# Performance work log

Hardware: AMD Instinct MI355X
Metric: run time of the kernel (lower is better)

## Reference

```python
import jax, jax.numpy as jnp
import numpy as np

MAX_RADIUS = 0.9
TEMP = 0.1

def _to_poincare(x, W, b):
    # Linear + Tanh, then rescale into Poincare ball of radius 0.9
    h = jnp.tanh(x @ W.T + b)
    norm = jnp.clip(jnp.linalg.norm(h, axis=-1, keepdims=True), 1e-8, None)
    scale = jnp.where(norm > MAX_RADIUS, MAX_RADIUS / norm, jnp.ones_like(norm))
    return h * scale

def setup_inputs() -> dict:
    key = jax.random.key(0)
    kq, kw, kb, km, ko = jax.random.split(key, 5)
    B, N, D = 2048, 100000, 128
    return {
        "query": jax.random.normal(kq, (B, D), dtype=jnp.float32),
        "W": jax.random.normal(kw, (D, D), dtype=jnp.float32) * (1.0 / np.sqrt(D)),
        "b": jax.random.normal(kb, (D,), dtype=jnp.float32) * 0.01,
        "mem_emb": jax.random.normal(km, (N, D), dtype=jnp.float32),
        "mem_out": jax.random.normal(ko, (N, D), dtype=jnp.float32),
        "k": 16,
    }

def reference(query, W, b, mem_emb, mem_out, k):
    q = _to_poincare(query, W, b)          # [B, D]
    m = _to_poincare(mem_emb, W, b)        # [N, D]
    # Euclidean cdist via the GEMM form: ||q||^2 + ||m||^2 - 2 q.m
    q2 = jnp.sum(q * q, axis=-1, keepdims=True)           # [B, 1]
    m2 = jnp.sum(m * m, axis=-1)                          # [N]
    d2 = q2 + m2[None, :] - 2.0 * (q @ m.T)               # [B, N]
    dists = jnp.sqrt(jnp.maximum(d2, 1e-12))
    # k smallest distances
    neg_top, top_idx = jax.lax.top_k(-dists, k)           # [B, k]
    top_dists = -neg_top
    weights = jax.nn.softmax(-top_dists / TEMP, axis=-1)  # [B, k]
    outcomes = mem_out[top_idx]                           # [B, k, D]
    return weights, outcomes
```

## Files before the change

### kernel.cpp

```cpp
#include <hip/hip_runtime.h>
#include <hip/hip_bf16.h>
#include <math.h>

#define DIM 128
#define QB 128
#define MB 64
#define NSPLIT 32
#define KSEL 16
#define KOWN 4
#define RESCORE 32
#define IDXMASK 0x1FFFu
#define KEYMASK 0xFFFFE000u
#define M2MAX 3200

using bf16x8 = __attribute__((ext_vector_type(8))) short;
using f32x4  = __attribute__((ext_vector_type(4))) float;

__device__ inline unsigned short f2bf(float f) {
  __hip_bfloat16 h = __float2bfloat16(f);
  return __builtin_bit_cast(unsigned short, h);
}
__device__ inline unsigned uminu(unsigned a, unsigned b) {
  return __builtin_elementwise_min(a, b);
}
__device__ inline unsigned umaxu(unsigned a, unsigned b) {
  return __builtin_elementwise_max(a, b);
}
__device__ inline unsigned umed3(unsigned a, unsigned b, unsigned c) {
  unsigned r;
  asm("v_med3_u32 %0, %1, %2, %3" : "=v"(r) : "v"(a), "v"(b), "v"(c));
  return r;
}
__device__ inline unsigned long long umin64(unsigned long long a,
                                            unsigned long long b) {
  return __builtin_elementwise_min(a, b);
}

__device__ inline f32x4 mfma16(bf16x8 a, bf16x8 b, f32x4 c) {
  return __builtin_amdgcn_mfma_f32_16x16x32_bf16(a, b, c, 0, 0, 0);
}

__device__ inline void gload_lds16(const void* g, void* l) {
  __builtin_amdgcn_global_load_lds(
      (const __attribute__((address_space(1))) void*)g,
      (__attribute__((address_space(3))) void*)l, 16, 0, 0);
}

__device__ inline void ins4(unsigned (&ks)[KOWN], unsigned c) {
  const unsigned n0 = uminu(c, ks[0]);
  const unsigned n1 = umed3(c, ks[0], ks[1]);
  const unsigned n2 = umed3(c, ks[1], ks[2]);
  const unsigned n3 = umed3(c, ks[2], ks[3]);
  ks[0] = n0; ks[1] = n1; ks[2] = n2; ks[3] = n3;
}

__global__ __launch_bounds__(512) void poincare2_k(
    const float* __restrict__ Xm, int Rm,
    const float* __restrict__ Xq, int Rq,
    const float* __restrict__ W, const float* __restrict__ bias,
    float* __restrict__ Pm, float* __restrict__ Pm2,
    float* __restrict__ Pm2s, int npadm,
    unsigned short* __restrict__ Pmbf,
    float* __restrict__ Pq, float* __restrict__ Pq2, int nbm)
{
  __shared__ float Wl[DIM * DIM];
  __shared__ float nrm[128 * 17];
  __shared__ float norm2l[128];

  const int t  = threadIdx.x;
  const int cg = t & 15;
  const int rg = t >> 4;

  const bool ismem = (int)blockIdx.x < nbm;
  const float* X = ismem ? Xm : Xq;
  const int    R = ismem ? Rm : Rq;
  float*       P  = ismem ? Pm  : Pq;
  float*       P2 = ismem ? Pm2 : Pq2;
  unsigned short* Pbf = ismem ? Pmbf : nullptr;
  const int rbase = (ismem ? blockIdx.x : (blockIdx.x - nbm)) * 128;

  for (int i = t; i < DIM * 32; i += 512) {
    const int j = i >> 5, c = i & 31;
    const float4 v = *(const float4*)&W[j * DIM + c * 4];
    *(float4*)&Wl[j * DIM + ((c ^ ((j >> 3) & 7)) << 2)] = v;
  }
  float bj[8];
  #pragma unroll
  for (int u = 0; u < 8; ++u) bj[u] = bias[cg * 8 + u];

  const float* xr[4];
  #pragma unroll
  for (int v = 0; v < 4; ++v) {
    int row = rbase + rg + 32 * v;
    if (row > R - 1) row = R - 1;
    xr[v] = X + (size_t)row * DIM;
  }
  __syncthreads();

  float acc[4][8];
  #pragma unroll
  for (int v = 0; v < 4; ++v)
    #pragma unroll
    for (int u = 0; u < 8; ++u) acc[v][u] = bj[u];

  #pragma unroll 2
  for (int k4 = 0; k4 < 32; ++k4) {
    float4 xv[4], wv[8];
    #pragma unroll
    for (int v = 0; v < 4; ++v) xv[v] = *(const float4*)&xr[v][k4 * 4];
    #pragma unroll
    for (int u = 0; u < 8; ++u) {
      const int j = cg * 8 + u;
      wv[u] = *(const float4*)&Wl[j * DIM + ((k4 ^ ((j >> 3) & 7)) << 2)];
    }
    #pragma unroll
    for (int v = 0; v < 4; ++v)
      #pragma unroll
      for (int u = 0; u < 8; ++u) {
        acc[v][u] = fmaf(xv[v].x, wv[u].x, acc[v][u]);
        acc[v][u] = fmaf(xv[v].y, wv[u].y, acc[v][u]);
        acc[v][u] = fmaf(xv[v].z, wv[u].z, acc[v][u]);
        acc[v][u] = fmaf(xv[v].w, wv[u].w, acc[v][u]);
      }
  }

  #pragma unroll
  for (int v = 0; v < 4; ++v) {
    float pn = 0.f;
    #pragma unroll
    for (int u = 0; u < 8; ++u) {
      const float th = tanhf(acc[v][u]);
      acc[v][u] = th;
      pn = fmaf(th, th, pn);
    }
    nrm[(rg + 32 * v) * 17 + cg] = pn;
  }
  __syncthreads();
  if (t < 128) {
    float s = 0.f;
    #pragma unroll
    for (int c2 = 0; c2 < 16; ++c2) s += nrm[t * 17 + c2];
    norm2l[t] = s;
    const int row = rbase + t;
    if (row < R) {
      const float nm = sqrtf(s);
      const float sc = (nm > 0.9f) ? (0.9f / nm) : 1.0f;
      const float p2v = s * sc * sc;
      P2[row] = p2v;
      if (ismem) Pm2s[row] = fmaf(0.5f, p2v, 1.0f);
    } else if (ismem && row < npadm) {
      Pm2s[row] = __int_as_float(0x7f800000);
    }
  }
  __syncthreads();

  #pragma unroll
  for (int v = 0; v < 4; ++v) {
    const int r = rg + 32 * v;
    const int row = rbase + r;
    if (row < R) {
      const float n2 = norm2l[r];
      const float nm = sqrtf(n2);
      const float sc = (nm > 0.9f) ? (0.9f / nm) : 1.0f;
      float o[8];
      #pragma unroll
      for (int u = 0; u < 8; ++u) o[u] = acc[v][u] * sc;
      *(float4*)&P[(size_t)row * DIM + cg * 8]     = make_float4(o[0], o[1], o[2], o[3]);
      *(float4*)&P[(size_t)row * DIM + cg * 8 + 4] = make_float4(o[4], o[5], o[6], o[7]);
      if (Pbf) {
        uint4 pb;
        pb.x = (unsigned)f2bf(o[0]) | ((unsigned)f2bf(o[1]) << 16);
        pb.y = (unsigned)f2bf(o[2]) | ((unsigned)f2bf(o[3]) << 16);
        pb.z = (unsigned)f2bf(o[4]) | ((unsigned)f2bf(o[5]) << 16);
        pb.w = (unsigned)f2bf(o[6]) | ((unsigned)f2bf(o[7]) << 16);
        *(uint4*)&Pmbf[(size_t)row * DIM + ((cg ^ (row & 15)) << 3)] = pb;
      }
    }
  }
}

template<bool USEBF>
__global__ __launch_bounds__(512, 2) void score_topk_k(
    const float* __restrict__ Pq,
    const float* __restrict__ Pm, const float* __restrict__ Pm2s,
    const unsigned short* __restrict__ Pmbf,
    int N, int splitlen, unsigned* __restrict__ splitTop)
{
  __shared__ __align__(16) unsigned short Ml[3][MB * DIM];
  __shared__ float m2all[M2MAX];

  const int t = threadIdx.x;
  const int lane = t & 63;
  const int w = t >> 6, wr = w >> 1, wc = w & 1;
  const int split = blockIdx.x;
  const int qbase = blockIdx.y * QB;
  const int mlo = split * splitlen;
  const int mhi = min(mlo + splitlen, N);
  const int ntiles = (mhi - mlo + MB - 1) / MB;

  bf16x8 qf[2][4];
  #pragma unroll
  for (int s = 0; s < 2; ++s) {
    const int qrow = qbase + wr * 32 + s * 16 + (lane & 15);
    #pragma unroll
    for (int ks = 0; ks < 4; ++ks) {
      const float* src = &Pq[(size_t)qrow * DIM + ks * 32 + (lane >> 4) * 8];
      float4 lo = *(const float4*)src;
      float4 hi = *(const float4*)(src + 4);
      bf16x8 v;
      v[0] = (short)f2bf(-lo.x); v[1] = (short)f2bf(-lo.y);
      v[2] = (short)f2bf(-lo.z); v[3] = (short)f2bf(-lo.w);
      v[4] = (short)f2bf(-hi.x); v[5] = (short)f2bf(-hi.y);
      v[6] = (short)f2bf(-hi.z); v[7] = (short)f2bf(-hi.w);
      qf[s][ks] = v;
    }
  }

  for (int i = t; i < splitlen; i += 512) m2all[i] = Pm2s[mlo + i];

  const size_t soff0 = (size_t)(w * 8 + (lane >> 4)) * DIM + ((lane & 15) << 3);
  const size_t soff1 = soff0 + 4 * DIM;

  auto stageU = [&](int tilei, int buf) {
    const unsigned short* b = Pmbf + (size_t)(mlo + tilei * MB) * DIM;
    gload_lds16(b + soff0, &Ml[buf][(w * 8) * DIM]);
    gload_lds16(b + soff1, &Ml[buf][(w * 8 + 4) * DIM]);
  };
  uint4 sv0, sv1;
  auto stageF_load = [&](int tilei) {
    const int fr = t >> 3, fe = t & 7;
    const float* src = Pm + (size_t)(mlo + tilei * MB + fr) * DIM + fe * 16;
    float4 a0 = *(const float4*)(src + 0);
    float4 a1 = *(const float4*)(src + 4);
    float4 a2 = *(const float4*)(src + 8);
    float4 a3 = *(const float4*)(src + 12);
    sv0.x = (unsigned)f2bf(a0.x) | ((unsigned)f2bf(a0.y) << 16);
    sv0.y = (unsigned)f2bf(a0.z) | ((unsigned)f2bf(a0.w) << 16);
    sv0.z = (unsigned)f2bf(a1.x) | ((unsigned)f2bf(a1.y) << 16);
    sv0.w = (unsigned)f2bf(a1.z) | ((unsigned)f2bf(a1.w) << 16);
    sv1.x = (unsigned)f2bf(a2.x) | ((unsigned)f2bf(a2.y) << 16);
    sv1.y = (unsigned)f2bf(a2.z) | ((unsigned)f2bf(a2.w) << 16);
    sv1.z = (unsigned)f2bf(a3.x) | ((unsigned)f2bf(a3.y) << 16);
    sv1.w = (unsigned)f2bf(a3.z) | ((unsigned)f2bf(a3.w) << 16);
  };
  auto stageF_write = [&](int buf) {
    const int fr = t >> 3, fe = t & 7;
    char* base = (char*)&Ml[buf][0] + fr * 256;
    *(uint4*)(base + (((2 * fe)     ^ (fr & 15)) << 4)) = sv0;
    *(uint4*)(base + (((2 * fe + 1) ^ (fr & 15)) << 4)) = sv1;
  };

  unsigned keys[2][4][KOWN];
  #pragma unroll
  for (int s = 0; s < 2; ++s)
    #pragma unroll
    for (int r = 0; r < 4; ++r)
      #pragma unroll
      for (int i = 0; i < KOWN; ++i) keys[s][r][i] = 0xFFFFFFFFu;

  const int mcol = wc * 32 + (lane & 15);
  const int rowA = mcol, rowB = mcol + 16;

  auto compute = [&](int tile, const unsigned short* cur) {
    const float ca = m2all[tile * MB + mcol];
    const float cb = m2all[tile * MB + mcol + 16];
    f32x4 a00 = (f32x4){ca, ca, ca, ca};
    f32x4 a01 = (f32x4){cb, cb, cb, cb};
    f32x4 a10 = (f32x4){ca, ca, ca, ca};
    f32x4 a11 = (f32x4){cb, cb, cb, cb};
    __builtin_amdgcn_s_setprio(1);
    #pragma unroll
    for (int ks = 0; ks < 4; ++ks) {
      const int kb = ks * 64 + (lane >> 4) * 16;
      bf16x8 bfrA = *(const bf16x8*)((const char*)cur + rowA * 256 +
                                     (kb ^ ((rowA & 15) << 4)));
      bf16x8 bfrB = *(const bf16x8*)((const char*)cur + rowB * 256 +
                                     (kb ^ ((rowB & 15) << 4)));
      a00 = mfma16(qf[0][ks], bfrA, a00);
      a01 = mfma16(qf[0][ks], bfrB, a01);
      a10 = mfma16(qf[1][ks], bfrA, a10);
      a11 = mfma16(qf[1][ks], bfrB, a11);
    }
    __builtin_amdgcn_s_setprio(0);
    const unsigned idx0 = (unsigned)(tile * MB + mcol);
    #pragma unroll
    for (int r = 0; r < 4; ++r) {
      ins4(keys[0][r], (__float_as_uint(a00[r]) & KEYMASK) | idx0);
      ins4(keys[0][r], (__float_as_uint(a01[r]) & KEYMASK) | (idx0 + 16));
      ins4(keys[1][r], (__float_as_uint(a10[r]) & KEYMASK) | idx0);
      ins4(keys[1][r], (__float_as_uint(a11[r]) & KEYMASK) | (idx0 + 16));
    }
  };

  if constexpr (USEBF) {
    __syncthreads();
    stageU(0, 0);
    if (ntiles > 1) stageU(1, 1);
    int cur = 0;
    for (int i = 0; i < ntiles; ++i) {
      if (i < ntiles - 1) asm volatile("s_waitcnt vmcnt(2)" ::: "memory");
      else                asm volatile("s_waitcnt vmcnt(0)" ::: "memory");
      __builtin_amdgcn_s_barrier();
      __builtin_amdgcn_sched_barrier(0);
      int nb = cur + 2; if (nb >= 3) nb -= 3;
      if (i + 2 < ntiles) stageU(i + 2, nb);
      compute(i, &Ml[cur][0]);
      cur = (cur + 1 == 3) ? 0 : cur + 1;
    }
  } else {
    stageF_load(0);
    stageF_write(0);
    __syncthreads();
    for (int i = 0; i < ntiles; ++i) {
      const int cur = i & 1;
      const bool more = (i + 1 < ntiles);
      if (more) stageF_load(i + 1);
      compute(i, &Ml[cur][0]);
      __syncthreads();
      if (more) stageF_write(cur ^ 1);
      __syncthreads();
    }
  }

  unsigned* mb = (unsigned*)&Ml[0][0];
  __syncthreads();
  #pragma unroll
  for (int s = 0; s < 2; ++s)
    #pragma unroll
    for (int r = 0; r < 4; ++r) {
      unsigned k0 = keys[s][r][0], k1 = keys[s][r][1];
      unsigned k2 = keys[s][r][2], k3 = keys[s][r][3];
      unsigned out = 0xFFFFFFFFu;
      for (int round = 0; round < 8; ++round) {
        unsigned g = k0;
        g = uminu(g, __shfl_xor(g, 1, 16));
        g = uminu(g, __shfl_xor(g, 2, 16));
        g = uminu(g, __shfl_xor(g, 4, 16));
        g = uminu(g, __shfl_xor(g, 8, 16));
        const bool mine = (k0 == g);
        k0 = mine ? k1 : k0;
        k1 = mine ? k2 : k1;
        k2 = mine ? k3 : k2;
        k3 = mine ? 0xFFFFFFFFu : k3;
        if ((lane & 15) == round) out = g;
      }
      const int lq = wr * 32 + s * 16 + (lane >> 4) * 4 + r;
      if ((lane & 15) < 8) mb[lq * 16 + wc * 8 + (lane & 15)] = out;
    }
  __syncthreads();
  if (wc == 0 && lane < 32) {
    const int lq = wr * 32 + lane;
    unsigned s8[8];
    #pragma unroll
    for (int i = 0; i < 8; ++i) s8[i] = 0xFFFFFFFFu;
    const unsigned* src = mb + lq * 16;
    #pragma unroll
    for (int i = 0; i < 16; ++i) {
      const unsigned c = src[i];
      const unsigned n0 = uminu(c, s8[0]);
      const unsigned n1 = umed3(c, s8[0], s8[1]);
      const unsigned n2 = umed3(c, s8[1], s8[2]);
      const unsigned n3 = umed3(c, s8[2], s8[3]);
      const unsigned n4 = umed3(c, s8[3], s8[4]);
      const unsigned n5 = umed3(c, s8[4], s8[5]);
      const unsigned n6 = umed3(c, s8[5], s8[6]);
      const unsigned n7 = umed3(c, s8[6], s8[7]);
      s8[0] = n0; s8[1] = n1; s8[2] = n2; s8[3] = n3;
      s8[4] = n4; s8[5] = n5; s8[6] = n6; s8[7] = n7;
    }
    unsigned* dst = &splitTop[((size_t)(qbase + lq) * NSPLIT + split) * 8];
    *(uint4*)dst       = make_uint4(s8[0], s8[1], s8[2], s8[3]);
    *((uint4*)dst + 1) = make_uint4(s8[4], s8[5], s8[6], s8[7]);
  }
}

__global__ __launch_bounds__(256) void finalize_k(
    const unsigned* __restrict__ splitTop,
    const float* __restrict__ Pq, const float* __restrict__ Pq2,
    const float* __restrict__ Pm, const float* __restrict__ Pm2,
    const float* __restrict__ memOut, int N, int splitlen,
    float* __restrict__ outW, float* __restrict__ outO)
{
  const int wv   = threadIdx.x >> 6;
  const int lane = threadIdx.x & 63;
  const int q = blockIdx.x * 4 + wv;

  __shared__ unsigned      sKey[4][RESCORE];
  __shared__ unsigned char sSrc[4][RESCORE];
  __shared__ unsigned long long sKeyx[4][RESCORE];
  __shared__ unsigned long long sSel[4][KSEL];
  __shared__ float sEl[4][KSEL];

  {
    unsigned a[8];
    if (lane < NSPLIT) {
      const unsigned* gp = splitTop + (size_t)q * (NSPLIT * 8) + lane * 8;
      uint4 lo = *(const uint4*)gp;
      uint4 hi = *(const uint4*)(gp + 4);
      a[0] = lo.x; a[1] = lo.y; a[2] = lo.z; a[3] = lo.w;
      a[4] = hi.x; a[5] = hi.y; a[6] = hi.z; a[7] = hi.w;
    } else {
      #pragma unroll
      for (int i = 0; i < 8; ++i) a[i] = 0xFFFFFFFFu;
    }
    for (int r = 0; r < RESCORE; ++r) {
      unsigned g = a[0];
      g = uminu(g, __shfl_xor(g, 1));
      g = uminu(g, __shfl_xor(g, 2));
      g = uminu(g, __shfl_xor(g, 4));
      g = uminu(g, __shfl_xor(g, 8));
      g = uminu(g, __shfl_xor(g, 16));
      g = uminu(g, __shfl_xor(g, 32));
      unsigned long long mask = __ballot(a[0] == g);
      const int fl = __ffsll((unsigned long long)mask) - 1;
      if (lane == fl) {
        #pragma unroll
        for (int i = 0; i < 7; ++i) a[i] = a[i + 1];
        a[7] = 0xFFFFFFFFu;
      }
      if (lane == 0) { sKey[wv][r] = g; sSrc[wv][r] = (unsigned char)fl; }
    }
  }

  #pragma unroll
  for (int p = 0; p < 4; ++p) {
    const int g8 = p * 8 + (lane >> 3), e = lane & 7;
    const int gidx = (int)sSrc[wv][g8] * splitlen + (int)(sKey[wv][g8] & IDXMASK);
    const float4* qr = (const float4*)&Pq[(size_t)q * DIM];
    const float4* mr = (const float4*)&Pm[(size_t)gidx * DIM];
    float s = 0.f;
    #pragma unroll
    for (int u = 0; u < 4; ++u) {
      float4 a = qr[e * 4 + u], b = mr[e * 4 + u];
      s = fmaf(a.x, b.x, s); s = fmaf(a.y, b.y, s);
      s = fmaf(a.z, b.z, s); s = fmaf(a.w, b.w, s);
    }
    s += __shfl_xor(s, 1, 8);
    s += __shfl_xor(s, 2, 8);
    s += __shfl_xor(s, 4, 8);
    if (e == 0) {
      float d2 = (Pq2[q] + Pm2[gidx]) - 2.0f * s;
      float dist = sqrtf(fmaxf(d2, 1e-12f));
      sKeyx[wv][g8] =
          (((unsigned long long)__float_as_uint(dist)) << 32) | (unsigned)gidx;
    }
  }

  {
    unsigned long long kk = (lane < RESCORE) ? sKeyx[wv][lane] : ~0ull;
    for (int r = 0; r < KSEL; ++r) {
      unsigned long long g = kk;
      g = umin64(g, __shfl_xor(g, 1));
      g = umin64(g, __shfl_xor(g, 2));
      g = umin64(g, __shfl_xor(g, 4));
      g = umin64(g, __shfl_xor(g, 8));
      g = umin64(g, __shfl_xor(g, 16));
      g = umin64(g, __shfl_xor(g, 32));
      if (kk == g) kk = ~0ull;
      if (lane == 0) sSel[wv][r] = g;
    }
  }

  if (lane < KSEL) {
    const float d  = __uint_as_float((unsigned)(sSel[wv][lane] >> 32));
    const float d0 = __uint_as_float((unsigned)(sSel[wv][0] >> 32));
    sEl[wv][lane] = expf((d0 - d) * 10.0f);
  }
  if (lane < KSEL) {
    float sum = 0.f;
    #pragma unroll
    for (int i = 0; i < KSEL; ++i) sum += sEl[wv][i];
    outW[(size_t)q * KSEL + lane] = sEl[wv][lane] / sum;
  }

  #pragma unroll
  for (int i = 0; i < 8; ++i) {
    const int f4 = lane + i * 64;
    const int r = f4 >> 5, c4 = f4 & 31;
    const int idx = (int)(sSel[wv][r] & 0xffffffffu);
    *(float4*)&outO[((size_t)q * KSEL + r) * DIM + c4 * 4] =
        *(const float4*)&memOut[(size_t)idx * DIM + c4 * 4];
  }
}

extern "C" void kernel_launch(void* const* d_in, const int* in_sizes, int n_in,
                              void* d_out, int out_size, void* d_ws, size_t ws_size,
                              hipStream_t stream)
{
  const float* query   = (const float*)d_in[0];
  const float* W       = (const float*)d_in[1];
  const float* bias    = (const float*)d_in[2];
  const float* mem_emb = (const float*)d_in[3];
  const float* mem_out = (const float*)d_in[4];
  const int B = in_sizes[0] / DIM;
  const int N = in_sizes[3] / DIM;

  const int splitlen = ((N + NSPLIT * MB - 1) / (NSPLIT * MB)) * MB;
  const int N_pad2 = NSPLIT * splitlen;

  float* ws  = (float*)d_ws;
  float* Pm  = ws;
  float* Pm2 = Pm + (size_t)N * DIM;
  float* Pm2s = Pm2 + N;
  float* Pq  = Pm2s + N_pad2;
  float* Pq2 = Pq + (size_t)B * DIM;
  unsigned* splitTop = (unsigned*)(Pq2 + B);
  unsigned short* Pmbf = (unsigned short*)(splitTop + (size_t)B * NSPLIT * 8);
  const size_t need_bf = (size_t)((char*)(Pmbf + (size_t)N_pad2 * DIM) - (char*)d_ws);
  const bool usebf = ws_size >= need_bf;

  float* outW = (float*)d_out;
  float* outO = outW + (size_t)B * KSEL;

  const int nbm = (N_pad2 + 127) / 128;
  const int nbq = (B + 127) / 128;
  poincare2_k<<<dim3(nbm + nbq), dim3(512), 0, stream>>>(
      mem_emb, N, query, B, W, bias, Pm, Pm2, Pm2s, N_pad2,
      usebf ? Pmbf : nullptr, Pq, Pq2, nbm);

  dim3 grid2(NSPLIT, B / QB);
  if (usebf)
    score_topk_k<true><<<grid2, dim3(512), 0, stream>>>(Pq, Pm, Pm2s, Pmbf, N,
                                                        splitlen, splitTop);
  else
    score_topk_k<false><<<grid2, dim3(512), 0, stream>>>(Pq, Pm, Pm2s, nullptr, N,
                                                         splitlen, splitTop);

  finalize_k<<<dim3(B / 4), dim3(256), 0, stream>>>(splitTop, Pq, Pq2, Pm, Pm2,
                                                    mem_out, N, splitlen,
                                                    outW, outO);
}
```

Baseline: 191.3 us.

## Retile Poincare projection kernel to 256 rows per block with shuffle norm reduction

Result: slower. 225.2 us (+17.8%).

```diff
diff --git a/kernel.cpp b/kernel.cpp
--- a/kernel.cpp
+++ b/kernel.cpp
@@ -54,7 +54,7 @@
   ks[0] = n0; ks[1] = n1; ks[2] = n2; ks[3] = n3;
 }
 
-__global__ __launch_bounds__(512) void poincare2_k(
+__global__ __launch_bounds__(512, 2) void poincare2_k(
     const float* __restrict__ Xm, int Rm,
     const float* __restrict__ Xq, int Rq,
     const float* __restrict__ W, const float* __restrict__ bias,
@@ -64,12 +64,10 @@
     float* __restrict__ Pq, float* __restrict__ Pq2, int nbm)
 {
   __shared__ float Wl[DIM * DIM];
-  __shared__ float nrm[128 * 17];
-  __shared__ float norm2l[128];
-
-  const int t  = threadIdx.x;
-  const int cg = t & 15;
-  const int rg = t >> 4;
+
+  const int t   = threadIdx.x;
+  const int cg  = t & 15;
+  const int rg2 = t >> 4;
 
   const bool ismem = (int)blockIdx.x < nbm;
   const float* X = ismem ? Xm : Xq;
@@ -77,94 +75,92 @@
   float*       P  = ismem ? Pm  : Pq;
   float*       P2 = ismem ? Pm2 : Pq2;
   unsigned short* Pbf = ismem ? Pmbf : nullptr;
-  const int rbase = (ismem ? blockIdx.x : (blockIdx.x - nbm)) * 128;
+  const int rbase = (ismem ? blockIdx.x : (blockIdx.x - nbm)) * 256;
+  const int r0 = rbase + rg2 * 8;
 
   for (int i = t; i < DIM * 32; i += 512) {
     const int j = i >> 5, c = i & 31;
     const float4 v = *(const float4*)&W[j * DIM + c * 4];
     *(float4*)&Wl[j * DIM + ((c ^ ((j >> 3) & 7)) << 2)] = v;
   }
-  float bj[8];
-  #pragma unroll
-  for (int u = 0; u < 8; ++u) bj[u] = bias[cg * 8 + u];
-
-  const float* xr[4];
-  #pragma unroll
-  for (int v = 0; v < 4; ++v) {
-    int row = rbase + rg + 32 * v;
-    if (row > R - 1) row = R - 1;
-    xr[v] = X + (size_t)row * DIM;
-  }
+
+  unsigned xoff[8];
+  #pragma unroll
+  for (int i = 0; i < 8; ++i) {
+    int row = r0 + i; if (row > R - 1) row = R - 1;
+    xoff[i] = (unsigned)row * (DIM * 4);
+  }
+
+  float acc[8][8];
+  #pragma unroll
+  for (int i = 0; i < 8; ++i)
+    #pragma unroll
+    for (int u = 0; u < 8; ++u) acc[i][u] = bias[cg * 8 + u];
   __syncthreads();
 
-  float acc[4][8];
-  #pragma unroll
-  for (int v = 0; v < 4; ++v)
-    #pragma unroll
-    for (int u = 0; u < 8; ++u) acc[v][u] = bj[u];
-
+  const float* Wb = &Wl[(cg * 8) * DIM];
+  const int sw = (cg & 7) << 2;
   #pragma unroll 2
   for (int k4 = 0; k4 < 32; ++k4) {
-    float4 xv[4], wv[8];
-    #pragma unroll
-    for (int v = 0; v < 4; ++v) xv[v] = *(const float4*)&xr[v][k4 * 4];
+    float4 xv[8];
+    #pragma unroll
+    for (int i = 0; i < 8; ++i)
+      xv[i] = *(const float4*)((const char*)X + xoff[i] + k4 * 16);
+    const int wch = ((k4 << 2) ^ sw);
     #pragma unroll
     for (int u = 0; u < 8; ++u) {
-      const int j = cg * 8 + u;
-      wv[u] = *(const float4*)&Wl[j * DIM + ((k4 ^ ((j >> 3) & 7)) << 2)];
-    }
-    #pragma unroll
-    for (int v = 0; v < 4; ++v)
+      const float4 wvv = *(const float4*)(Wb + u * DIM + wch);
       #pragma unroll
-      for (int u = 0; u < 8; ++u) {
-        acc[v][u] = fmaf(xv[v].x, wv[u].x, acc[v][u]);
-        acc[v][u] = fmaf(xv[v].y, wv[u].y, acc[v][u]);
-        acc[v][u] = fmaf(xv[v].z, wv[u].z, acc[v][u]);
-        acc[v][u] = fmaf(xv[v].w, wv[u].w, acc[v][u]);
+      for (int i = 0; i < 8; ++i) {
+        acc[i][u] = fmaf(xv[i].x, wvv.x, acc[i][u]);
+        acc[i][u] = fmaf(xv[i].y, wvv.y, acc[i][u]);
+        acc[i][u] = fmaf(xv[i].z, wvv.z, acc[i][u]);
+        acc[i][u] = fmaf(xv[i].w, wvv.w, acc[i][u]);
       }
-  }
-
-  #pragma unroll
-  for (int v = 0; v < 4; ++v) {
-    float pn = 0.f;
+    }
+  }
+
+  float pn[8];
+  #pragma unroll
+  for (int i = 0; i < 8; ++i) {
+    float p = 0.f;
     #pragma unroll
     for (int u = 0; u < 8; ++u) {
-      const float th = tanhf(acc[v][u]);
-      acc[v][u] = th;
-      pn = fmaf(th, th, pn);
-    }
-    nrm[(rg + 32 * v) * 17 + cg] = pn;
-  }
-  __syncthreads();
-  if (t < 128) {
-    float s = 0.f;
-    #pragma unroll
-    for (int c2 = 0; c2 < 16; ++c2) s += nrm[t * 17 + c2];
-    norm2l[t] = s;
-    const int row = rbase + t;
+      acc[i][u] = tanhf(acc[i][u]);
+      p = fmaf(acc[i][u], acc[i][u], p);
+    }
+    p += __shfl_xor(p, 1, 16);
+    p += __shfl_xor(p, 2, 16);
+    p += __shfl_xor(p, 4, 16);
+    p += __shfl_xor(p, 8, 16);
+    pn[i] = p;
+  }
+
+  if (cg == 0) {
+    #pragma unroll
+    for (int i = 0; i < 8; ++i) {
+      const int row = r0 + i;
+      if (row < R) {
+        const float nm = sqrtf(pn[i]);
+        const float sc = (nm > 0.9f) ? (0.9f / nm) : 1.0f;
+        const float p2v = pn[i] * sc * sc;
+        P2[row] = p2v;
+        if (ismem) Pm2s[row] = fmaf(0.5f, p2v, 1.0f);
+      } else if (ismem && row < npadm) {
+        Pm2s[row] = __int_as_float(0x7f800000);
+      }
+    }
+  }
+
+  #pragma unroll
+  for (int i = 0; i < 8; ++i) {
+    const int row = r0 + i;
     if (row < R) {
-      const float nm = sqrtf(s);
-      const float sc = (nm > 0.9f) ? (0.9f / nm) : 1.0f;
-      const float p2v = s * sc * sc;
-      P2[row] = p2v;
-      if (ismem) Pm2s[row] = fmaf(0.5f, p2v, 1.0f);
-    } else if (ismem && row < npadm) {
-      Pm2s[row] = __int_as_float(0x7f800000);
-    }
-  }
-  __syncthreads();
-
-  #pragma unroll
-  for (int v = 0; v < 4; ++v) {
-    const int r = rg + 32 * v;
-    const int row = rbase + r;
-    if (row < R) {
-      const float n2 = norm2l[r];
-      const float nm = sqrtf(n2);
+      const float nm = sqrtf(pn[i]);
       const float sc = (nm > 0.9f) ? (0.9f / nm) : 1.0f;
       float o[8];
       #pragma unroll
-      for (int u = 0; u < 8; ++u) o[u] = acc[v][u] * sc;
+      for (int u = 0; u < 8; ++u) o[u] = acc[i][u] * sc;
       *(float4*)&P[(size_t)row * DIM + cg * 8]     = make_float4(o[0], o[1], o[2], o[3]);
       *(float4*)&P[(size_t)row * DIM + cg * 8 + 4] = make_float4(o[4], o[5], o[6], o[7]);
       if (Pbf) {
@@ -512,8 +508,8 @@
   float* outW = (float*)d_out;
   float* outO = outW + (size_t)B * KSEL;
 
-  const int nbm = (N_pad2 + 127) / 128;
-  const int nbq = (B + 127) / 128;
+  const int nbm = N_pad2 / 256;
+  const int nbq = B / 256;
   poincare2_k<<<dim3(nbm + nbq), dim3(512), 0, stream>>>(
       mem_emb, N, query, B, W, bias, Pm, Pm2, Pm2s, N_pad2,
       usebf ? Pmbf : nullptr, Pq, Pq2, nbm);
```
